# Optimization experiments

Hardware: AMD Instinct MI355X
Metric: run time of the kernel (lower is better)

Reference implementation:

```python
import jax, jax.numpy as jnp
import numpy as np
from jax import lax

EPS = 1e-12  # F.normalize default eps


def setup_inputs() -> dict:
    key = jax.random.key(0)
    ks = jax.random.split(key, 4)
    b, dim, h, w = 8, 192, 128, 128
    num_heads = 6
    x = jax.random.normal(ks[0], (b, dim, h, w), dtype=jnp.float32)
    y = jax.random.normal(ks[1], (b, dim, h, w), dtype=jnp.float32)
    # depthwise conv weight (groups = 3*dim): [3*dim, 1, 3, 3]
    w_dw = jax.random.normal(ks[2], (3 * dim, 1, 3, 3), dtype=jnp.float32) * 0.1
    # 1x1 projection: [dim, dim]
    w_proj = jax.random.normal(ks[3], (dim, dim), dtype=jnp.float32) * (1.0 / np.sqrt(dim))
    temperature = jnp.ones((num_heads, 1, 1), dtype=jnp.float32)
    return {"x": x, "y": y, "w_dw": w_dw, "w_proj": w_proj,
            "temperature": temperature, "num_heads": num_heads}


def _l2norm(t):
    n = jnp.sqrt(jnp.sum(t * t, axis=-1, keepdims=True))
    return t / jnp.maximum(n, EPS)


def reference(x, y, w_dw, w_proj, temperature, num_heads):
    b, c, h, w = x.shape
    qkv_in = jnp.concatenate([x, y, y], axis=1)  # [b, 3c, h, w]
    # depthwise 3x3 conv, stride 1, padding 1 (groups = 3c)
    qkv = lax.conv_general_dilated(
        qkv_in, w_dw, window_strides=(1, 1), padding=((1, 1), (1, 1)),
        dimension_numbers=("NCHW", "OIHW", "NCHW"), feature_group_count=3 * c)
    q, k, v = jnp.split(qkv, 3, axis=1)
    ch = c // num_heads
    rs = lambda t: t.reshape(b, num_heads, ch, h * w)  # b head c (h w)
    q, k, v = rs(q), rs(k), rs(v)
    q = _l2norm(q)
    k = _l2norm(k)
    # channel attention: [b, head, ch, ch]
    attn = jnp.einsum("bhcn,bhdn->bhcd", q, k) * temperature
    attn = jax.nn.softmax(attn, axis=-1)
    out = jnp.einsum("bhcd,bhdn->bhcn", attn, v).reshape(b, c, h, w)
    # 1x1 conv projection
    out = jnp.einsum("oc,bchw->bohw", w_proj, out)
    return out
```

## Files before the change

### kernel.cpp

```cpp
#include <hip/hip_runtime.h>
#include <hip/hip_bf16.h>

#define DEV __device__ __forceinline__

typedef unsigned short u16;
typedef unsigned int u32;
typedef __attribute__((ext_vector_type(8))) short short8;
typedef __attribute__((ext_vector_type(4))) float f32x4;

DEV u16 f2bf(float f) {
  __hip_bfloat16 h = __float2bfloat16(f);
  return *(u16*)&h;
}
DEV float bf2f_s(short s) { return __uint_as_float(((u32)(u16)s) << 16); }

#define NB 8
#define NH 6
#define CTOT 192
#define HW 16384
#define VTS 34

__global__ __launch_bounds__(256) void kconv(
    const float* __restrict__ x, const float* __restrict__ y,
    const float* __restrict__ wdw,
    u16* __restrict__ qws, u16* __restrict__ kws, u16* __restrict__ vws)
{
  const int t = threadIdx.x, lane = t & 63, w = t >> 6;
  int task = blockIdx.x * 4 + w;
  const int iskv = (task >= 6144) ? 1 : 0;
  if (iskv) task -= 6144;
  const int b   = task / 768;
  const int rem = task - b * 768;
  const int gc  = rem >> 2;
  const int rg  = rem & 3;
  const int r0  = rg * 32;

  const float* __restrict__ in =
      (iskv ? y : x) + (((size_t)(b * CTOT + gc)) << 14);

  float w0[9], w1[9];
  if (!iskv) {
#pragma unroll
    for (int i = 0; i < 9; ++i) w0[i] = wdw[gc * 9 + i];
  } else {
#pragma unroll
    for (int i = 0; i < 9; ++i) {
      w0[i] = wdw[(CTOT + gc) * 9 + i];
      w1[i] = wdw[(2 * CTOT + gc) * 9 + i];
    }
  }

  u16* __restrict__ out0 =
      (iskv ? kws : qws) + (((size_t)(b * CTOT + gc)) << 14);
  u16* __restrict__ out1 = vws + (((size_t)(b * CTOT + gc)) << 14);

  #define LOADRAW(ar) ((ar) >= 0 && (ar) < 128 \
      ? *(const float2*)(in + (ar) * 128 + lane * 2) \
      : make_float2(0.f, 0.f))
  #define SHUF(v, dst) { \
      float lf = __shfl_up((v).y, 1);  if (lane == 0)  lf = 0.f; \
      float rt = __shfl_down((v).x, 1); if (lane == 63) rt = 0.f; \
      (dst) = make_float4(lf, (v).x, (v).y, rt); }

  float4 ring[4];
  float2 raw[2];
  { float2 v = LOADRAW(r0 - 1); SHUF(v, ring[0]); }
  { float2 v = LOADRAW(r0);     SHUF(v, ring[1]); }
  raw[1] = LOADRAW(r0 + 1);

  for (int r8 = 0; r8 < 8; ++r8) {
#pragma unroll
    for (int j = 0; j < 4; ++j) {
      const int r = r0 + r8 * 4 + j;
      raw[j & 1] = LOADRAW(r + 2);
      SHUF(raw[(j + 1) & 1], ring[(j + 2) & 3]);
      const float4 rm = ring[j & 3];
      const float4 rc = ring[(j + 1) & 3];
      const float4 rp = ring[(j + 2) & 3];

      float o0, o1;
      o0 = w0[0] * rm.x; o0 = fmaf(w0[1], rm.y, o0); o0 = fmaf(w0[2], rm.z, o0);
      o0 = fmaf(w0[3], rc.x, o0); o0 = fmaf(w0[4], rc.y, o0); o0 = fmaf(w0[5], rc.z, o0);
      o0 = fmaf(w0[6], rp.x, o0); o0 = fmaf(w0[7], rp.y, o0); o0 = fmaf(w0[8], rp.z, o0);
      o1 = w0[0] * rm.y; o1 = fmaf(w0[1], rm.z, o1); o1 = fmaf(w0[2], rm.w, o1);
      o1 = fmaf(w0[3], rc.y, o1); o1 = fmaf(w0[4], rc.z, o1); o1 = fmaf(w0[5], rc.w, o1);
      o1 = fmaf(w0[6], rp.y, o1); o1 = fmaf(w0[7], rp.z, o1); o1 = fmaf(w0[8], rp.w, o1);
      ((u32*)(out0 + r * 128))[lane] = ((u32)f2bf(o1) << 16) | (u32)f2bf(o0);

      if (iskv) {
        float v0, v1;
        v0 = w1[0] * rm.x; v0 = fmaf(w1[1], rm.y, v0); v0 = fmaf(w1[2], rm.z, v0);
        v0 = fmaf(w1[3], rc.x, v0); v0 = fmaf(w1[4], rc.y, v0); v0 = fmaf(w1[5], rc.z, v0);
        v0 = fmaf(w1[6], rp.x, v0); v0 = fmaf(w1[7], rp.y, v0); v0 = fmaf(w1[8], rp.z, v0);
        v1 = w1[0] * rm.y; v1 = fmaf(w1[1], rm.z, v1); v1 = fmaf(w1[2], rm.w, v1);
        v1 = fmaf(w1[3], rc.y, v1); v1 = fmaf(w1[4], rc.z, v1); v1 = fmaf(w1[5], rc.w, v1);
        v1 = fmaf(w1[6], rp.y, v1); v1 = fmaf(w1[7], rp.z, v1); v1 = fmaf(w1[8], rp.w, v1);
        ((u32*)(out1 + r * 128))[lane] = ((u32)f2bf(v1) << 16) | (u32)f2bf(v0);
      }
    }
  }
  #undef LOADRAW
  #undef SHUF
}

__global__ __launch_bounds__(256) void k2a_gram(
    const u16* __restrict__ qws, const u16* __restrict__ kws,
    float* __restrict__ gram, float* __restrict__ sqq, float* __restrict__ sqk)
{
  const int t = threadIdx.x, l = t & 63, w = t >> 6;
  const int bh = blockIdx.x >> 4, tile = blockIdx.x & 15;
  const int p0 = tile * 1024 + w * 256;
  const u16* qb = qws + (((size_t)bh) << 19);
  const u16* kb = kws + (((size_t)bh) << 19);
  const int row = l & 15;
  const int kq  = (l >> 4) * 8;

  f32x4 acc[2][2] = {};
  float sq[2] = {0.f, 0.f}, sk[2] = {0.f, 0.f};

  for (int ks = 0; ks < 8; ++ks) {
    const int p = p0 + ks * 32 + kq;
    short8 av[2], bv[2];
#pragma unroll
    for (int tc = 0; tc < 2; ++tc) {
      av[tc] = *(const short8*)(qb + (((size_t)(tc * 16 + row)) << 14) + p);
      bv[tc] = *(const short8*)(kb + (((size_t)(tc * 16 + row)) << 14) + p);
    }
#pragma unroll
    for (int tc = 0; tc < 2; ++tc) {
#pragma unroll
      for (int j = 0; j < 8; ++j) {
        float fa = bf2f_s(av[tc][j]); sq[tc] = fmaf(fa, fa, sq[tc]);
        float fb = bf2f_s(bv[tc][j]); sk[tc] = fmaf(fb, fb, sk[tc]);
      }
    }
#pragma unroll
    for (int tc = 0; tc < 2; ++tc)
#pragma unroll
      for (int td = 0; td < 2; ++td)
        acc[tc][td] = __builtin_amdgcn_mfma_f32_16x16x32_bf16(av[tc], bv[td], acc[tc][td], 0, 0, 0);
  }

#pragma unroll
  for (int tc = 0; tc < 2; ++tc)
#pragma unroll
    for (int td = 0; td < 2; ++td)
#pragma unroll
      for (int rr = 0; rr < 4; ++rr) {
        int c = tc * 16 + (l >> 4) * 4 + rr;
        int d = td * 16 + row;
        atomicAdd(gram + (size_t)bh * 1024 + c * 32 + d, acc[tc][td][rr]);
      }

#pragma unroll
  for (int tc = 0; tc < 2; ++tc) {
    sq[tc] += __shfl_xor(sq[tc], 16);
    sq[tc] += __shfl_xor(sq[tc], 32);
    sk[tc] += __shfl_xor(sk[tc], 16);
    sk[tc] += __shfl_xor(sk[tc], 32);
  }
  if ((l >> 4) == 0) {
#pragma unroll
    for (int tc = 0; tc < 2; ++tc) {
      atomicAdd(sqq + bh * 32 + tc * 16 + row, sq[tc]);
      atomicAdd(sqk + bh * 32 + tc * 16 + row, sk[tc]);
    }
  }
}

__global__ __launch_bounds__(256) void k2b_w2(
    const float* __restrict__ gram, const float* __restrict__ sqq,
    const float* __restrict__ sqk, const float* __restrict__ wp,
    const float* __restrict__ temp, u16* __restrict__ W2)
{
  __shared__ float Ls[32][33];
  __shared__ float As[32][33];
  __shared__ float wl[192 * 32];
  __shared__ float nq[32], nk[32];
  const int t = threadIdx.x;
  const int bh = blockIdx.x, b = bh / 6, h = bh % 6;
  const float tmp = temp[h];
  if (t < 32) nq[t] = fmaxf(sqrtf(sqq[bh * 32 + t]), 1e-12f);
  else if (t < 64) nk[t - 32] = fmaxf(sqrtf(sqk[bh * 32 + t - 32]), 1e-12f);
  __syncthreads();
#pragma unroll
  for (int i = 0; i < 4; ++i) {
    int idx = i * 256 + t, c = idx >> 5, d = idx & 31;
    Ls[c][d] = gram[(size_t)bh * 1024 + idx] / (nq[c] * nk[d]) * tmp;
  }
  __syncthreads();
  if (t < 32) {
    float m = -1e30f;
#pragma unroll
    for (int d = 0; d < 32; ++d) m = fmaxf(m, Ls[t][d]);
    float s = 0.f;
#pragma unroll
    for (int d = 0; d < 32; ++d) s += expf(Ls[t][d] - m);
    float inv = 1.0f / s;
#pragma unroll
    for (int d = 0; d < 32; ++d) As[t][d] = expf(Ls[t][d] - m) * inv;
  }
  for (int i = 0; i < 24; ++i) {
    int idx = i * 256 + t, o = idx >> 5, c = idx & 31;
    wl[idx] = wp[o * 192 + h * 32 + c];
  }
  __syncthreads();
  for (int i = 0; i < 24; ++i) {
    int idx = i * 256 + t, o = idx >> 5, d = idx & 31;
    float a = 0.f;
#pragma unroll
    for (int c = 0; c < 32; ++c) a = fmaf(wl[o * 32 + c], As[c][d], a);
    W2[((size_t)(b * 192 + o)) * 192 + h * 32 + d] = f2bf(a);
  }
}

__global__ __launch_bounds__(256) void k3_gemm(
    const u16* __restrict__ W2, const u16* __restrict__ vnat,
    float* __restrict__ out)
{
  __shared__ __align__(16) u16 b_tile[128 * VTS];
  __shared__ __align__(16) float cout[32 * 132];
  const int t = threadIdx.x, l = t & 63, w = t >> 6;
  const int bx = blockIdx.x;
  const int b  = bx >> 7, nb = bx & 127;
  const int arow = l & 15;
  const int kq8  = (l >> 4) * 8;
  const u16* w2b = W2 + (size_t)b * 192 * 192;
  const u16* vb  = vnat + ((size_t)b * CTOT) * HW;
  const int n0 = nb * 128;

  f32x4 acc[12][2] = {};

  for (int ks = 0; ks < 6; ++ks) {
    if (ks > 0) __syncthreads();
#pragma unroll
    for (int r2 = 0; r2 < 2; ++r2) {
      const int ch   = (t >> 4) + r2 * 16;
      const int nseg = (t & 15) * 8;
      short8 vv = *(const short8*)(vb + (size_t)(ks * 32 + ch) * HW + n0 + nseg);
#pragma unroll
      for (int j = 0; j < 8; ++j) b_tile[(nseg + j) * VTS + ch] = (u16)vv[j];
    }
    __syncthreads();

    short8 bf[2];
#pragma unroll
    for (int nt = 0; nt < 2; ++nt)
      bf[nt] = *(const short8*)&b_tile[(w * 32 + nt * 16 + arow) * VTS + kq8];
#pragma unroll
    for (int ot = 0; ot < 12; ++ot) {
      short8 af = *(const short8*)(w2b + (size_t)(ot * 16 + arow) * 192 + ks * 32 + kq8);
#pragma unroll
      for (int nt = 0; nt < 2; ++nt)
        acc[ot][nt] = __builtin_amdgcn_mfma_f32_16x16x32_bf16(af, bf[nt], acc[ot][nt], 0, 0, 0);
    }
  }

  float* __restrict__ ob = out + ((size_t)b * 192) * 16384;
#pragma unroll
  for (int og = 0; og < 6; ++og) {
    __syncthreads();
#pragma unroll
    for (int oi = 0; oi < 2; ++oi) {
#pragma unroll
      for (int nt = 0; nt < 2; ++nt)
#pragma unroll
        for (int rr = 0; rr < 4; ++rr) {
          const int o_l = oi * 16 + (l >> 4) * 4 + rr;
          const int n_l = w * 32 + nt * 16 + (l & 15);
          cout[o_l * 132 + n_l] = acc[og * 2 + oi][nt][rr];
        }
    }
    __syncthreads();
    const int o_l = t >> 3;
    const int o   = og * 32 + o_l;
#pragma unroll
    for (int c = 0; c < 4; ++c) {
      const int n = (t & 7) * 4 + c * 32;
      float4 v4;
      v4.x = cout[o_l * 132 + n + 0];
      v4.y = cout[o_l * 132 + n + 1];
      v4.z = cout[o_l * 132 + n + 2];
      v4.w = cout[o_l * 132 + n + 3];
      *(float4*)(ob + (size_t)o * 16384 + n0 + n) = v4;
    }
  }
}

extern "C" void kernel_launch(void* const* d_in, const int* in_sizes, int n_in,
                              void* d_out, int out_size, void* d_ws, size_t ws_size,
                              hipStream_t stream)
{
  const float* x    = (const float*)d_in[0];
  const float* y    = (const float*)d_in[1];
  const float* wdw  = (const float*)d_in[2];
  const float* wp   = (const float*)d_in[3];
  const float* temp = (const float*)d_in[4];

  char* ws = (char*)d_ws;
  const size_t QK = (size_t)NB * CTOT * HW * 2;
  u16*   qws  = (u16*)(ws);
  u16*   kws  = (u16*)(ws + QK);
  u16*   vws  = (u16*)(ws + 2 * QK);
  float* gram = (float*)(ws + 3 * QK);
  float* sqq  = (float*)(ws + 3 * QK + 196608);
  float* sqk  = (float*)(ws + 3 * QK + 196608 + 6144);
  u16*   W2   = (u16*)(ws + 3 * QK + 196608 + 12288);
  float* out  = (float*)d_out;

  hipMemsetAsync(ws + 3 * QK, 0, 208896, stream);
  kconv<<<3072, 256, 0, stream>>>(x, y, wdw, qws, kws, vws);
  k2a_gram<<<768, 256, 0, stream>>>(qws, kws, gram, sqq, sqk);
  k2b_w2<<<48, 256, 0, stream>>>(gram, sqq, sqk, wp, temp, W2);
  k3_gemm<<<1024, 256, 0, stream>>>(W2, vws, out);
}
```

Before: 174.5 us.

## Stage depthwise conv input tiles in LDS with 4-wide outputs per thread

The depthwise 3x3 conv kernel now loads a 66x128 halo tile per block into shared memory using float4 global loads. It then computes four adjacent outputs per thread from LDS instead of streaming rows through registers with wave shuffles. Blocks are remapped so each one handles half of one channel image, with q and kv blocks interleaved, and the grid doubles. This aims to widen global loads and stores and remove the shuffle traffic, at the cost of a block-wide barrier and about 35 KB of LDS per block, which may reduce occupancy.

```diff
diff --git a/kernel.cpp b/kernel.cpp
--- a/kernel.cpp
+++ b/kernel.cpp
@@ -19,21 +19,23 @@
 #define CTOT 192
 #define HW 16384
 #define VTS 34
+#define LSTR 136
 
 __global__ __launch_bounds__(256) void kconv(
     const float* __restrict__ x, const float* __restrict__ y,
     const float* __restrict__ wdw,
     u16* __restrict__ qws, u16* __restrict__ kws, u16* __restrict__ vws)
 {
+  __shared__ __align__(16) float lds[66 * LSTR];
   const int t = threadIdx.x, lane = t & 63, w = t >> 6;
-  int task = blockIdx.x * 4 + w;
-  const int iskv = (task >= 6144) ? 1 : 0;
-  if (iskv) task -= 6144;
-  const int b   = task / 768;
-  const int rem = task - b * 768;
-  const int gc  = rem >> 2;
-  const int rg  = rem & 3;
-  const int r0  = rg * 32;
+  const int bx   = blockIdx.x;
+  const int iskv = bx & 1;
+  const int rest = bx >> 1;
+  const int chp  = rest & 1;
+  const int task = rest >> 1;
+  const int b  = task / 192;
+  const int gc = task % 192;
+  const int r0 = chp * 64;
 
   const float* __restrict__ in =
       (iskv ? y : x) + (((size_t)(b * CTOT + gc)) << 14);
@@ -50,57 +52,76 @@
     }
   }
 
+  if (t < 132) {
+    const int row = t >> 1;
+    lds[row * LSTR + ((t & 1) ? 132 : 3)] = 0.f;
+  }
+#pragma unroll
+  for (int i = 0; i < 9; ++i) {
+    const int idx = i * 256 + t;
+    if (idx < 2112) {
+      const int row = idx >> 5, c4 = idx & 31;
+      const int grow = r0 - 1 + row;
+      float4 v = (grow >= 0 && grow < 128)
+          ? *(const float4*)(in + grow * 128 + c4 * 4)
+          : make_float4(0.f, 0.f, 0.f, 0.f);
+      *(float4*)&lds[row * LSTR + 4 + c4 * 4] = v;
+    }
+  }
+  __syncthreads();
+
+  const int j    = lane & 31;
+  const int half = lane >> 5;
   u16* __restrict__ out0 =
       (iskv ? kws : qws) + (((size_t)(b * CTOT + gc)) << 14);
   u16* __restrict__ out1 = vws + (((size_t)(b * CTOT + gc)) << 14);
 
-  #define LOADRAW(ar) ((ar) >= 0 && (ar) < 128 \
-      ? *(const float2*)(in + (ar) * 128 + lane * 2) \
-      : make_float2(0.f, 0.f))
-  #define SHUF(v, dst) { \
-      float lf = __shfl_up((v).y, 1);  if (lane == 0)  lf = 0.f; \
-      float rt = __shfl_down((v).x, 1); if (lane == 63) rt = 0.f; \
-      (dst) = make_float4(lf, (v).x, (v).y, rt); }
-
-  float4 ring[4];
-  float2 raw[2];
-  { float2 v = LOADRAW(r0 - 1); SHUF(v, ring[0]); }
-  { float2 v = LOADRAW(r0);     SHUF(v, ring[1]); }
-  raw[1] = LOADRAW(r0 + 1);
-
-  for (int r8 = 0; r8 < 8; ++r8) {
-#pragma unroll
-    for (int j = 0; j < 4; ++j) {
-      const int r = r0 + r8 * 4 + j;
-      raw[j & 1] = LOADRAW(r + 2);
-      SHUF(raw[(j + 1) & 1], ring[(j + 2) & 3]);
-      const float4 rm = ring[j & 3];
-      const float4 rc = ring[(j + 1) & 3];
-      const float4 rp = ring[(j + 2) & 3];
-
-      float o0, o1;
-      o0 = w0[0] * rm.x; o0 = fmaf(w0[1], rm.y, o0); o0 = fmaf(w0[2], rm.z, o0);
-      o0 = fmaf(w0[3], rc.x, o0); o0 = fmaf(w0[4], rc.y, o0); o0 = fmaf(w0[5], rc.z, o0);
-      o0 = fmaf(w0[6], rp.x, o0); o0 = fmaf(w0[7], rp.y, o0); o0 = fmaf(w0[8], rp.z, o0);
-      o1 = w0[0] * rm.y; o1 = fmaf(w0[1], rm.z, o1); o1 = fmaf(w0[2], rm.w, o1);
-      o1 = fmaf(w0[3], rc.y, o1); o1 = fmaf(w0[4], rc.z, o1); o1 = fmaf(w0[5], rc.w, o1);
-      o1 = fmaf(w0[6], rp.y, o1); o1 = fmaf(w0[7], rp.z, o1); o1 = fmaf(w0[8], rp.w, o1);
-      ((u32*)(out0 + r * 128))[lane] = ((u32)f2bf(o1) << 16) | (u32)f2bf(o0);
-
-      if (iskv) {
-        float v0, v1;
-        v0 = w1[0] * rm.x; v0 = fmaf(w1[1], rm.y, v0); v0 = fmaf(w1[2], rm.z, v0);
-        v0 = fmaf(w1[3], rc.x, v0); v0 = fmaf(w1[4], rc.y, v0); v0 = fmaf(w1[5], rc.z, v0);
-        v0 = fmaf(w1[6], rp.x, v0); v0 = fmaf(w1[7], rp.y, v0); v0 = fmaf(w1[8], rp.z, v0);
-        v1 = w1[0] * rm.y; v1 = fmaf(w1[1], rm.z, v1); v1 = fmaf(w1[2], rm.w, v1);
-        v1 = fmaf(w1[3], rc.y, v1); v1 = fmaf(w1[4], rc.z, v1); v1 = fmaf(w1[5], rc.w, v1);
-        v1 = fmaf(w1[6], rp.y, v1); v1 = fmaf(w1[7], rp.z, v1); v1 = fmaf(w1[8], rp.w, v1);
-        ((u32*)(out1 + r * 128))[lane] = ((u32)f2bf(v1) << 16) | (u32)f2bf(v0);
+#pragma unroll
+  for (int i = 0; i < 8; ++i) {
+    const int lrow = w * 16 + i * 2 + half;
+    const int r = r0 + lrow;
+
+    float  lt[3], rt[3];
+    float4 md[3];
+#pragma unroll
+    for (int dr = 0; dr < 3; ++dr) {
+      const int base = (lrow + dr) * LSTR + 4 * j;
+      lt[dr] = lds[base + 3];
+      md[dr] = *(const float4*)&lds[base + 4];
+      rt[dr] = lds[base + 8];
+    }
+
+    {
+      float o0 = 0.f, o1 = 0.f, o2 = 0.f, o3 = 0.f;
+#pragma unroll
+      for (int dr = 0; dr < 3; ++dr) {
+        const float a = lt[dr], b0 = md[dr].x, c = md[dr].y,
+                    d = md[dr].z, e = md[dr].w, f = rt[dr];
+        o0 = fmaf(w0[dr * 3 + 0], a,  o0); o0 = fmaf(w0[dr * 3 + 1], b0, o0); o0 = fmaf(w0[dr * 3 + 2], c, o0);
+        o1 = fmaf(w0[dr * 3 + 0], b0, o1); o1 = fmaf(w0[dr * 3 + 1], c,  o1); o1 = fmaf(w0[dr * 3 + 2], d, o1);
+        o2 = fmaf(w0[dr * 3 + 0], c,  o2); o2 = fmaf(w0[dr * 3 + 1], d,  o2); o2 = fmaf(w0[dr * 3 + 2], e, o2);
+        o3 = fmaf(w0[dr * 3 + 0], d,  o3); o3 = fmaf(w0[dr * 3 + 1], e,  o3); o3 = fmaf(w0[dr * 3 + 2], f, o3);
       }
-    }
-  }
-  #undef LOADRAW
-  #undef SHUF
+      const u32 p01 = ((u32)f2bf(o1) << 16) | (u32)f2bf(o0);
+      const u32 p23 = ((u32)f2bf(o3) << 16) | (u32)f2bf(o2);
+      *(uint2*)(out0 + r * 128 + 4 * j) = make_uint2(p01, p23);
+    }
+    if (iskv) {
+      float o0 = 0.f, o1 = 0.f, o2 = 0.f, o3 = 0.f;
+#pragma unroll
+      for (int dr = 0; dr < 3; ++dr) {
+        const float a = lt[dr], b0 = md[dr].x, c = md[dr].y,
+                    d = md[dr].z, e = md[dr].w, f = rt[dr];
+        o0 = fmaf(w1[dr * 3 + 0], a,  o0); o0 = fmaf(w1[dr * 3 + 1], b0, o0); o0 = fmaf(w1[dr * 3 + 2], c, o0);
+        o1 = fmaf(w1[dr * 3 + 0], b0, o1); o1 = fmaf(w1[dr * 3 + 1], c,  o1); o1 = fmaf(w1[dr * 3 + 2], d, o1);
+        o2 = fmaf(w1[dr * 3 + 0], c,  o2); o2 = fmaf(w1[dr * 3 + 1], d,  o2); o2 = fmaf(w1[dr * 3 + 2], e, o2);
+        o3 = fmaf(w1[dr * 3 + 0], d,  o3); o3 = fmaf(w1[dr * 3 + 1], e,  o3); o3 = fmaf(w1[dr * 3 + 2], f, o3);
+      }
+      const u32 p01 = ((u32)f2bf(o1) << 16) | (u32)f2bf(o0);
+      const u32 p23 = ((u32)f2bf(o3) << 16) | (u32)f2bf(o2);
+      *(uint2*)(out1 + r * 128 + 4 * j) = make_uint2(p01, p23);
+    }
+  }
 }
 
 __global__ __launch_bounds__(256) void k2a_gram(
@@ -309,7 +330,7 @@
   float* out  = (float*)d_out;
 
   hipMemsetAsync(ws + 3 * QK, 0, 208896, stream);
-  kconv<<<3072, 256, 0, stream>>>(x, y, wdw, qws, kws, vws);
+  kconv<<<6144, 256, 0, stream>>>(x, y, wdw, qws, kws, vws);
   k2a_gram<<<768, 256, 0, stream>>>(qws, kws, gram, sqq, sqk);
   k2b_w2<<<48, 256, 0, stream>>>(gram, sqq, sqk, wp, temp, W2);
   k3_gemm<<<1024, 256, 0, stream>>>(W2, vws, out);
```

Result: no change. 174.4 us (-0.1%).
